# Performance work log

Measured on AMD Instinct MI355X. Metric: run time of the kernel, lower is better.

Reference implementation:

```python
import jax, jax.numpy as jnp
import numpy as np

N = 100000
E = 1600000
IN_DIM = 128
HID_DIM = 128
OUT_DIM = 128


def _gcn_conv(x, W, b, row, col, n):
    # PyG GCNConv: x' = D^{-1/2} (A + I) D^{-1/2} (x W) + b, self-loops included
    xw = x @ W  # [n, dout]
    deg = jnp.zeros((n,), xw.dtype).at[col].add(1.0)  # in-degree incl self-loops
    dinv = jnp.where(deg > 0, jax.lax.rsqrt(deg), 0.0)
    norm = dinv[row] * dinv[col]  # [e]
    msg = xw[row] * norm[:, None]  # [e, dout] -- dominant memory traffic
    out = jax.ops.segment_sum(msg, col, num_segments=n)
    return out + b


def setup_inputs() -> dict:
    key = jax.random.key(0)
    k1, k2, k3, k4, k5, k6 = jax.random.split(key, 6)
    posts = jax.random.normal(k1, (N, IN_DIM), dtype=jnp.float32)
    edge_index = jax.random.randint(k2, (2, E), 0, N, dtype=jnp.int64)
    W1 = jax.random.normal(k3, (IN_DIM, HID_DIM), dtype=jnp.float32) * (1.0 / np.sqrt(IN_DIM))
    b1 = jnp.zeros((HID_DIM,), dtype=jnp.float32)
    W2 = jax.random.normal(k4, (HID_DIM + IN_DIM, OUT_DIM), dtype=jnp.float32) * (1.0 / np.sqrt(HID_DIM + IN_DIM))
    b2 = jnp.zeros((OUT_DIM,), dtype=jnp.float32)
    return {"posts": posts, "W1": W1, "b1": b1, "W2": W2, "b2": b2,
            "edge_index": edge_index, "rootIndex": 0}


def reference(posts, W1, b1, W2, b2, edge_index, rootIndex):
    n = posts.shape[0]
    loops = jnp.arange(n, dtype=edge_index.dtype)
    row = jnp.concatenate([edge_index[0], loops])
    col = jnp.concatenate([edge_index[1], loops])

    conv1_out = _gcn_conv(posts, W1, b1, row, col, n)  # [n, hid]
    post_root = jnp.broadcast_to(posts[rootIndex], (n, posts.shape[1]))
    conv1_root = jnp.broadcast_to(conv1_out[rootIndex], (n, conv1_out.shape[1]))

    conv2_in = jax.nn.relu(jnp.concatenate([conv1_out, post_root], axis=1))
    # dropout is identity at inference
    conv2_out = jax.nn.relu(_gcn_conv(conv2_in, W2, b2, row, col, n))

    feature = jnp.concatenate([conv1_root, conv2_out], axis=1)  # [n, hid+out]
    # avg_pool1d(kernel_size=3, stride=1) over the feature axis -> [n, hid+out-2]
    pooled = (feature[:, :-2] + feature[:, 1:-1] + feature[:, 2:]) * (1.0 / 3.0)
    return pooled
```

## Files before the change

### kernel.cpp

```cpp
#include <hip/hip_runtime.h>
#include <hip/hip_fp16.h>

#define DIM 128
typedef _Float16 half8 __attribute__((ext_vector_type(8)));
typedef float f32x4 __attribute__((ext_vector_type(4)));

__global__ void k_scan1(const int* __restrict__ cnt, int* __restrict__ off,
                        int* __restrict__ bsum, int N){
  __shared__ int s[256];
  int i = blockIdx.x*256 + threadIdx.x;
  int v = (i < N) ? cnt[i] : 0;
  s[threadIdx.x] = v;
  __syncthreads();
  for (int d = 1; d < 256; d <<= 1){
    int t = (threadIdx.x >= d) ? s[threadIdx.x - d] : 0;
    __syncthreads();
    s[threadIdx.x] += t;
    __syncthreads();
  }
  if (i < N) off[i] = s[threadIdx.x] - v;
  if (threadIdx.x == 255) bsum[blockIdx.x] = s[255];
}

__global__ void k_scan2(int* __restrict__ bsum, int nb){
  __shared__ int s[512];
  int t = threadIdx.x;
  int v = (t < nb) ? bsum[t] : 0;
  s[t] = v;
  __syncthreads();
  for (int d = 1; d < 512; d <<= 1){
    int x = (t >= d) ? s[t - d] : 0;
    __syncthreads();
    s[t] += x;
    __syncthreads();
  }
  if (t < nb) bsum[t] = s[t] - v;
}

__global__ void k_scan3(int* __restrict__ off, const int* __restrict__ bsum,
                        const int* __restrict__ cnt, float* __restrict__ dinv,
                        __half* __restrict__ dinvh, int N){
  int i = blockIdx.x*blockDim.x + threadIdx.x;
  if (i < N){
    off[i] += bsum[i >> 8];
    float d = rsqrtf((float)(cnt[i] + 1));
    dinv[i] = d;
    dinvh[i] = __float2half_rn(d);
  }
}

#define NSTRIPE 8
__global__ void k_scatter(const int* __restrict__ row, const int* __restrict__ col,
                          const int* __restrict__ rank, const int* __restrict__ off,
                          int* __restrict__ csr_row, int E, int N){
  int stride = gridDim.x * 256;
  for (int s = 0; s < NSTRIPE; s++){
    int lo = (int)(((long long)s * N) >> 3);
    int hi = (int)(((long long)(s+1) * N) >> 3);
    for (int e = blockIdx.x*256 + threadIdx.x; e < E; e += stride){
      int c = col[e];
      if (c >= lo && c < hi){
        csr_row[off[c] + rank[e]] = row[e];
      }
    }
  }
}

__global__ void k_wprep(const float* __restrict__ Wsrc, __half* __restrict__ Wfh){
  _Float16* Wf = (_Float16*)Wfh;
  int id   = blockIdx.x*256 + threadIdx.x;
  int lane = id & 63;
  int ckc  = id >> 6;
  int kc   = ckc & 3, ct = ckc >> 2;
  int kbase = kc*32 + (lane >> 4)*8;
  int c     = ct*16 + (lane & 15);
  half8 v;
  #pragma unroll
  for (int i = 0; i < 8; i++)
    v[i] = (_Float16)Wsrc[(size_t)(kbase + i)*DIM + c];
  *(half8*)(Wf + (size_t)id*8) = v;
}

template<int INH>
__device__ __forceinline__ void gemm_mfma(const void* __restrict__ Xv,
    const _Float16* __restrict__ Wf, const float* __restrict__ addvec,
    const float* __restrict__ dinv, __half* __restrict__ Yh, int N, int doRelu, int gb){
  int wid = threadIdx.x >> 6;
  int l   = threadIdx.x & 63;
  int g   = l >> 4;
  int lr  = l & 15;
  int rowA = gb*64 + wid*16 + lr;
  int rA   = (rowA < N) ? rowA : (N - 1);

  f32x4 acc[8];
  #pragma unroll
  for (int ct = 0; ct < 8; ct++) acc[ct] = (f32x4){0.f, 0.f, 0.f, 0.f};

  #pragma unroll
  for (int kc = 0; kc < 4; kc++){
    half8 a;
    if (INH){
      a = *(const half8*)((const _Float16*)Xv + (size_t)rA*DIM + kc*32 + g*8);
    } else {
      const float* xp = (const float*)Xv + (size_t)rA*DIM + kc*32 + g*8;
      float4 x0 = *(const float4*)xp;
      float4 x1 = *(const float4*)(xp + 4);
      a[0]=(_Float16)x0.x; a[1]=(_Float16)x0.y; a[2]=(_Float16)x0.z; a[3]=(_Float16)x0.w;
      a[4]=(_Float16)x1.x; a[5]=(_Float16)x1.y; a[6]=(_Float16)x1.z; a[7]=(_Float16)x1.w;
    }
    if (doRelu){
      #pragma unroll
      for (int i = 0; i < 8; i++) a[i] = (a[i] > (_Float16)0.f) ? a[i] : (_Float16)0.f;
    }
    #pragma unroll
    for (int ct = 0; ct < 8; ct++){
      half8 b = *(const half8*)(Wf + ((size_t)(ct*4 + kc)*64 + l)*8);
      acc[ct] = __builtin_amdgcn_mfma_f32_16x16x32_f16(a, b, acc[ct], 0, 0, 0);
    }
  }

  int m0 = gb*64 + wid*16 + g*4;
  float av[8];
  #pragma unroll
  for (int ct = 0; ct < 8; ct++) av[ct] = addvec ? addvec[ct*16 + lr] : 0.f;
  #pragma unroll
  for (int r = 0; r < 4; r++){
    int rr = m0 + r;
    if (rr < N){
      float dv = dinv ? dinv[rr] : 1.f;
      #pragma unroll
      for (int ct = 0; ct < 8; ct++){
        float o = dv*(acc[ct][r] + av[ct]);
        Yh[(size_t)rr*DIM + ct*16 + lr] = __float2half(o);
      }
    }
  }
}

template<int INH>
__global__ __launch_bounds__(256) void k_gemmM(const void* __restrict__ Xv,
    const __half* __restrict__ Wfh, const float* __restrict__ addvec,
    const float* __restrict__ dinv, __half* __restrict__ Yh, int N, int doRelu){
  gemm_mfma<INH>(Xv, (const _Float16*)Wfh, addvec, dinv, Yh, N, doRelu, blockIdx.x);
}

__global__ __launch_bounds__(256) void k_megaA(const float* __restrict__ posts,
    const __half* __restrict__ Wf1, __half* __restrict__ xw1u,
    const int* __restrict__ col, int E, int* __restrict__ cnt, int* __restrict__ rank,
    int N, int nG, int nC){
  int bid = blockIdx.x;
  int m = bid % 5;
  if (m == 4){
    int g = bid / 5;
    if (g < nG)
      gemm_mfma<0>(posts, (const _Float16*)Wf1, nullptr, nullptr, xw1u, N, 0, g);
  } else {
    int c = (bid/5)*4 + m;
    if (c < nC){
      int i = c*256 + threadIdx.x;
      if (i < E) rank[i] = atomicAdd(&cnt[col[i]], 1);
    }
  }
}

__global__ void k_conv1(const __half* __restrict__ xw1u, const int* __restrict__ csr_row,
                        const int* __restrict__ off, const int* __restrict__ cnt,
                        const float* __restrict__ dinv, const __half* __restrict__ dinvh,
                        const float* __restrict__ b, const int* __restrict__ rootIdx,
                        __half* __restrict__ outh, float* __restrict__ c1root, int N){
  int wid  = (blockIdx.x*blockDim.x + threadIdx.x) >> 6;
  if (wid >= N) return;
  int lane = threadIdx.x & 63;
  int half = lane >> 5;
  int sl   = lane & 31;
  int v = wid;
  float dv = dinv[v];
  int o0 = off[v], total = cnt[v] + 1;

  __half2 a01 = __float2half2_rn(0.f), a23 = __float2half2_rn(0.f);
  const __half* base = xw1u;

  auto idx = [&](int t){ return (t == 0) ? v : csr_row[o0 + t - 1]; };
  auto accum = [&](uint2 wv, __half dh){
    __half2 d2 = __half2half2(dh);
    a01 = __hfma2(*(__half2*)&wv.x, d2, a01);
    a23 = __hfma2(*(__half2*)&wv.y, d2, a23);
  };

  int j = half;
  if (j + 14 < total){
    int nid[8];
    #pragma unroll
    for (int q = 0; q < 8; q++) nid[q] = idx(j + 2*q);
    while (j + 14 < total){
      int cur[8];
      #pragma unroll
      for (int q = 0; q < 8; q++) cur[q] = nid[q];
      int jn = j + 16;
      if (jn + 14 < total){
        #pragma unroll
        for (int q = 0; q < 8; q++) nid[q] = csr_row[o0 + jn + 2*q - 1];
      }
      uint2 u[8]; __half dh[8];
      #pragma unroll
      for (int q = 0; q < 8; q++){
        u[q]  = *(const uint2*)(base + (size_t)cur[q]*DIM + sl*4);
        dh[q] = dinvh[cur[q]];
      }
      #pragma unroll
      for (int q = 0; q < 8; q++) accum(u[q], dh[q]);
      j = jn;
    }
  }
  while (j + 6 < total){
    int i0 = idx(j), i1 = idx(j+2), i2 = idx(j+4), i3 = idx(j+6);
    uint2 u0 = *(const uint2*)(base + (size_t)i0*DIM + sl*4);
    uint2 u1 = *(const uint2*)(base + (size_t)i1*DIM + sl*4);
    uint2 u2 = *(const uint2*)(base + (size_t)i2*DIM + sl*4);
    uint2 u3 = *(const uint2*)(base + (size_t)i3*DIM + sl*4);
    __half d0 = dinvh[i0], d1 = dinvh[i1], d2 = dinvh[i2], d3 = dinvh[i3];
    accum(u0, d0); accum(u1, d1); accum(u2, d2); accum(u3, d3);
    j += 8;
  }
  for (; j < total; j += 2){
    int r = idx(j);
    uint2 u = *(const uint2*)(base + (size_t)r*DIM + sl*4);
    accum(u, dinvh[r]);
  }

  int r01 = __shfl_xor(*(int*)&a01, 32);
  int r23 = __shfl_xor(*(int*)&a23, 32);
  a01 = __hadd2(a01, *(__half2*)&r01);
  a23 = __hadd2(a23, *(__half2*)&r23);

  if (half == 0){
    float2 f01 = __half22float2(a01), f23 = __half22float2(a23);
    float4 bb = *(const float4*)(b + sl*4);
    float rx = dv*f01.x + bb.x, ry = dv*f01.y + bb.y;
    float rz = dv*f23.x + bb.z, rw = dv*f23.y + bb.w;
    __half2 h01 = __floats2half2_rn(rx, ry);
    __half2 h23 = __floats2half2_rn(rz, rw);
    uint2 u = make_uint2(*(unsigned int*)&h01, *(unsigned int*)&h23);
    *(uint2*)(outh + (size_t)v*DIM + sl*4) = u;
    if (v == rootIdx[0])
      *(float4*)(c1root + sl*4) = make_float4(rx, ry, rz, rw);
  }
}

__global__ void k_small(const float* __restrict__ posts, const float* __restrict__ W2,
                        const float* __restrict__ c1root, const int* __restrict__ rootIdx,
                        float* __restrict__ cvec, float* __restrict__ cpool){
  int j = threadIdx.x;
  int root = rootIdx[0];
  __shared__ float pr[DIM];
  __shared__ float cr[DIM];
  pr[j] = fmaxf(posts[(size_t)root*DIM + j], 0.f);
  cr[j] = c1root[j];
  __syncthreads();
  float s = 0.f;
  #pragma unroll 4
  for (int k = 0; k < DIM; k++) s += pr[k] * W2[(size_t)(DIM + k)*DIM + j];
  cvec[j] = s;
  cpool[j] = (j < 126) ? (cr[j] + cr[j+1] + cr[j+2]) * (1.f/3.f) : cr[j];
}

__global__ void k_conv2(const __half* __restrict__ xws, const int* __restrict__ csr_row,
                        const int* __restrict__ off, const int* __restrict__ cnt,
                        const float* __restrict__ dinv, const float* __restrict__ b2,
                        const float* __restrict__ cpool, float* __restrict__ out, int N){
  int wid  = (blockIdx.x*blockDim.x + threadIdx.x) >> 6;
  if (wid >= N) return;
  int lane = threadIdx.x & 63;
  int half = lane >> 5;
  int sl   = lane & 31;
  int v = wid;
  float dv = dinv[v];
  int o0 = off[v], total = cnt[v] + 1;

  __half2 a01 = __float2half2_rn(0.f), a23 = __float2half2_rn(0.f);
  const __half* base = xws;

  auto idx = [&](int t){ return (t == 0) ? v : csr_row[o0 + t - 1]; };
  auto accum = [&](uint2 wv){
    a01 = __hadd2(a01, *(__half2*)&wv.x);
    a23 = __hadd2(a23, *(__half2*)&wv.y);
  };

  int j = half;
  if (j + 14 < total){
    int nid[8];
    #pragma unroll
    for (int q = 0; q < 8; q++) nid[q] = idx(j + 2*q);
    while (j + 14 < total){
      int cur[8];
      #pragma unroll
      for (int q = 0; q < 8; q++) cur[q] = nid[q];
      int jn = j + 16;
      if (jn + 14 < total){
        #pragma unroll
        for (int q = 0; q < 8; q++) nid[q] = csr_row[o0 + jn + 2*q - 1];
      }
      uint2 u[8];
      #pragma unroll
      for (int q = 0; q < 8; q++) u[q] = *(const uint2*)(base + (size_t)cur[q]*DIM + sl*4);
      #pragma unroll
      for (int q = 0; q < 8; q++) accum(u[q]);
      j = jn;
    }
  }
  while (j + 6 < total){
    int i0 = idx(j), i1 = idx(j+2), i2 = idx(j+4), i3 = idx(j+6);
    uint2 u0 = *(const uint2*)(base + (size_t)i0*DIM + sl*4);
    uint2 u1 = *(const uint2*)(base + (size_t)i1*DIM + sl*4);
    uint2 u2 = *(const uint2*)(base + (size_t)i2*DIM + sl*4);
    uint2 u3 = *(const uint2*)(base + (size_t)i3*DIM + sl*4);
    accum(u0); accum(u1); accum(u2); accum(u3);
    j += 8;
  }
  for (; j < total; j += 2){
    uint2 u = *(const uint2*)(base + (size_t)idx(j)*DIM + sl*4);
    accum(u);
  }

  int r01 = __shfl_xor(*(int*)&a01, 32);
  int r23 = __shfl_xor(*(int*)&a23, 32);
  a01 = __hadd2(a01, *(__half2*)&r01);
  a23 = __hadd2(a23, *(__half2*)&r23);

  float2 f01 = __half22float2(a01), f23 = __half22float2(a23);
  float4 bb = *(const float4*)(b2 + sl*4);
  float o0v = fmaxf(dv*f01.x + bb.x, 0.f);
  float o1v = fmaxf(dv*f01.y + bb.y, 0.f);
  float o2v = fmaxf(dv*f23.x + bb.z, 0.f);
  float o3v = fmaxf(dv*f23.y + bb.w, 0.f);

  float pz = __shfl_up(o2v, 1);
  float pw = __shfl_up(o3v, 1);
  if (sl == 0){ pz = cpool[126]; pw = cpool[127]; }
  const float third = 1.f/3.f;
  float q0 = (pz + pw + o0v) * third;
  float q1 = (pw + o0v + o1v) * third;
  float q2 = (o0v + o1v + o2v) * third;
  float q3 = (o1v + o2v + o3v) * third;

  float* orow = out + (size_t)v*254;
  if (half == 0){
    *(float2*)(orow + 126 + sl*4)     = make_float2(q0, q1);
    *(float2*)(orow + 126 + sl*4 + 2) = make_float2(q2, q3);
  } else {
    if (sl < 31) *(float4*)(orow + sl*4) = *(const float4*)(cpool + sl*4);
    else         *(float2*)(orow + 124)  = *(const float2*)(cpool + 124);
  }
}

extern "C" void kernel_launch(void* const* d_in, const int* in_sizes, int n_in,
                              void* d_out, int out_size, void* d_ws, size_t ws_size,
                              hipStream_t stream){
  const float* posts = (const float*)d_in[0];
  const float* W1    = (const float*)d_in[1];
  const float* b1    = (const float*)d_in[2];
  const float* W2    = (const float*)d_in[3];
  const float* b2    = (const float*)d_in[4];
  const int*   eidx  = (const int*)d_in[5];
  const int*   rootI = (const int*)d_in[6];
  int N = in_sizes[0] / DIM;
  int E = in_sizes[5] / 2;
  const int* row = eidx;
  const int* col = eidx + E;

  char* p = (char*)d_ws;
  auto alloc = [&](size_t bytes)->void*{
    void* q = (void*)p; p += (bytes + 255) & ~(size_t)255; return q;
  };
  __half* xw1u  = (__half*)alloc((size_t)N*DIM*2);
  __half* xw2s  = (__half*)alloc((size_t)N*DIM*2);
  __half* c1h   = (__half*)alloc((size_t)N*DIM*2);
  __half* Wf1   = (__half*)alloc((size_t)DIM*DIM*2);
  __half* Wf2   = (__half*)alloc((size_t)DIM*DIM*2);
  __half* dinvh = (__half*)alloc((size_t)N*2);
  float* dinv   = (float*)alloc((size_t)N*4);
  float* c1root = (float*)alloc(DIM*4);
  float* cvec   = (float*)alloc(DIM*4);
  float* cpool  = (float*)alloc(DIM*4);
  int*   cnt    = (int*)alloc((size_t)N*4);
  int*   off    = (int*)alloc((size_t)N*4);
  int*   rank   = (int*)alloc((size_t)E*4);
  int*   bsum   = (int*)alloc(512*4);
  int*   csrrow = (int*)alloc((size_t)E*4);

  hipMemsetAsync(cnt, 0, (size_t)N*4, stream);

  int nb = (N + 255) / 256;
  int nG = (N + 63) / 64;
  int nC = (E + 255) / 256;
  int q5 = nG > (nC + 3)/4 ? nG : (nC + 3)/4;

  k_wprep<<<8, 256, 0, stream>>>(W1, Wf1);
  k_wprep<<<8, 256, 0, stream>>>(W2, Wf2);
  k_megaA<<<5*q5, 256, 0, stream>>>(posts, Wf1, xw1u, col, E, cnt, rank, N, nG, nC);
  k_scan1<<<nb, 256, 0, stream>>>(cnt, off, bsum, N);
  k_scan2<<<1, 512, 0, stream>>>(bsum, nb);
  k_scan3<<<nb, 256, 0, stream>>>(off, bsum, cnt, dinv, dinvh, N);
  k_scatter<<<2048, 256, 0, stream>>>(row, col, rank, off, csrrow, E, N);

  k_conv1<<<(N + 3)/4, 256, 0, stream>>>(xw1u, csrrow, off, cnt, dinv, dinvh, b1, rootI,
                                         c1h, c1root, N);
  k_small<<<1, 128, 0, stream>>>(posts, W2, c1root, rootI, cvec, cpool);
  k_gemmM<1><<<(N + 63)/64, 256, 0, stream>>>(c1h, Wf2, cvec, dinv, xw2s, N, 1);
  k_conv2<<<(N + 3)/4, 256, 0, stream>>>(xw2s, csrrow, off, cnt, dinv, b2, cpool,
                                         (float*)d_out, N);
}
```

Measured before the change: 293.9 us.

## Fuse layer-1 GEMM with CSR scatter instead of with degree counting

Separates the atomic degree count into its own kernel and moves the first-layer MFMA GEMM into a combined kernel with the CSR scatter. The idea is to overlap the compute-bound GEMM with the memory-bound scatter rather than with the atomics, so the GEMM blocks come first and the scatter blocks fill in around them. The scatter also drops from 8 column stripes to 4, cutting passes over the edge list but giving each pass a wider write window and less locality. The count kernel now stands alone on the critical path.

```diff
diff --git a/kernel.cpp b/kernel.cpp
--- a/kernel.cpp
+++ b/kernel.cpp
@@ -4,6 +4,12 @@
 #define DIM 128
 typedef _Float16 half8 __attribute__((ext_vector_type(8)));
 typedef float f32x4 __attribute__((ext_vector_type(4)));
+
+__global__ void k_count(const int* __restrict__ col, int E,
+                        int* __restrict__ cnt, int* __restrict__ rank){
+  int i = blockIdx.x*blockDim.x + threadIdx.x;
+  if (i < E) rank[i] = atomicAdd(&cnt[col[i]], 1);
+}
 
 __global__ void k_scan1(const int* __restrict__ cnt, int* __restrict__ off,
                         int* __restrict__ bsum, int N){
@@ -46,23 +52,6 @@
     float d = rsqrtf((float)(cnt[i] + 1));
     dinv[i] = d;
     dinvh[i] = __float2half_rn(d);
-  }
-}
-
-#define NSTRIPE 8
-__global__ void k_scatter(const int* __restrict__ row, const int* __restrict__ col,
-                          const int* __restrict__ rank, const int* __restrict__ off,
-                          int* __restrict__ csr_row, int E, int N){
-  int stride = gridDim.x * 256;
-  for (int s = 0; s < NSTRIPE; s++){
-    int lo = (int)(((long long)s * N) >> 3);
-    int hi = (int)(((long long)(s+1) * N) >> 3);
-    for (int e = blockIdx.x*256 + threadIdx.x; e < E; e += stride){
-      int c = col[e];
-      if (c >= lo && c < hi){
-        csr_row[off[c] + rank[e]] = row[e];
-      }
-    }
   }
 }
 
@@ -144,21 +133,28 @@
   gemm_mfma<INH>(Xv, (const _Float16*)Wfh, addvec, dinv, Yh, N, doRelu, blockIdx.x);
 }
 
-__global__ __launch_bounds__(256) void k_megaA(const float* __restrict__ posts,
+#define NSTRIPE 4
+__global__ __launch_bounds__(256) void k_megaB(const float* __restrict__ posts,
     const __half* __restrict__ Wf1, __half* __restrict__ xw1u,
-    const int* __restrict__ col, int E, int* __restrict__ cnt, int* __restrict__ rank,
-    int N, int nG, int nC){
+    const int* __restrict__ row, const int* __restrict__ col,
+    const int* __restrict__ rank, const int* __restrict__ off,
+    int* __restrict__ csr_row, int E, int N, int nG, int nS){
   int bid = blockIdx.x;
-  int m = bid % 5;
-  if (m == 4){
-    int g = bid / 5;
-    if (g < nG)
-      gemm_mfma<0>(posts, (const _Float16*)Wf1, nullptr, nullptr, xw1u, N, 0, g);
+  if (bid < nG){
+    gemm_mfma<0>(posts, (const _Float16*)Wf1, nullptr, nullptr, xw1u, N, 0, bid);
   } else {
-    int c = (bid/5)*4 + m;
-    if (c < nC){
-      int i = c*256 + threadIdx.x;
-      if (i < E) rank[i] = atomicAdd(&cnt[col[i]], 1);
+    int sb = bid - nG;
+    int stride = nS * 256;
+    #pragma unroll 1
+    for (int s = 0; s < NSTRIPE; s++){
+      int lo = (int)(((long long)s * N) / NSTRIPE);
+      int hi = (int)(((long long)(s+1) * N) / NSTRIPE);
+      for (int e = sb*256 + threadIdx.x; e < E; e += stride){
+        int c = col[e];
+        if (c >= lo && c < hi){
+          csr_row[off[c] + rank[e]] = row[e];
+        }
+      }
     }
   }
 }
@@ -392,16 +388,16 @@
 
   int nb = (N + 255) / 256;
   int nG = (N + 63) / 64;
-  int nC = (E + 255) / 256;
-  int q5 = nG > (nC + 3)/4 ? nG : (nC + 3)/4;
+  int nS = 2048;
 
   k_wprep<<<8, 256, 0, stream>>>(W1, Wf1);
   k_wprep<<<8, 256, 0, stream>>>(W2, Wf2);
-  k_megaA<<<5*q5, 256, 0, stream>>>(posts, Wf1, xw1u, col, E, cnt, rank, N, nG, nC);
+  k_count<<<(E + 255)/256, 256, 0, stream>>>(col, E, cnt, rank);
   k_scan1<<<nb, 256, 0, stream>>>(cnt, off, bsum, N);
   k_scan2<<<1, 512, 0, stream>>>(bsum, nb);
   k_scan3<<<nb, 256, 0, stream>>>(off, bsum, cnt, dinv, dinvh, N);
-  k_scatter<<<2048, 256, 0, stream>>>(row, col, rank, off, csrrow, E, N);
+  k_megaB<<<nG + nS, 256, 0, stream>>>(posts, Wf1, xw1u, row, col, rank, off,
+                                       csrrow, E, N, nG, nS);
 
   k_conv1<<<(N + 3)/4, 256, 0, stream>>>(xw1u, csrrow, off, cnt, dinv, dinvh, b1, rootI,
                                          c1h, c1root, N);
```

After: 309.7 us. +5.4%, slower.

## Cache scatter positions, merge weight prep, move constant pooled columns into GEMM kernel

Applied to the files above, without the earlier changes.

The CSR scatter now computes each edge's destination position once, stores it in a new pos buffer, and filters later stripes by position range instead of re-reading col, off and rank. The two weight-prep launches are merged into one. Writing the constant first 126 output columns (cpool) moves out of conv2 into extra blocks of a new combined kernel alongside the second GEMM. This trades an extra E-sized buffer and a less coalesced column fill for fewer launches and less per-stripe gather traffic, and it shortens conv2's epilogue.

```diff
diff --git a/kernel.cpp b/kernel.cpp
--- a/kernel.cpp
+++ b/kernel.cpp
@@ -52,23 +52,33 @@
 #define NSTRIPE 8
 __global__ void k_scatter(const int* __restrict__ row, const int* __restrict__ col,
                           const int* __restrict__ rank, const int* __restrict__ off,
-                          int* __restrict__ csr_row, int E, int N){
+                          int* __restrict__ pos, int* __restrict__ csr_row, int E, int N){
   int stride = gridDim.x * 256;
-  for (int s = 0; s < NSTRIPE; s++){
-    int lo = (int)(((long long)s * N) >> 3);
-    int hi = (int)(((long long)(s+1) * N) >> 3);
-    for (int e = blockIdx.x*256 + threadIdx.x; e < E; e += stride){
-      int c = col[e];
-      if (c >= lo && c < hi){
-        csr_row[off[c] + rank[e]] = row[e];
-      }
-    }
-  }
-}
-
-__global__ void k_wprep(const float* __restrict__ Wsrc, __half* __restrict__ Wfh){
-  _Float16* Wf = (_Float16*)Wfh;
-  int id   = blockIdx.x*256 + threadIdx.x;
+  int tid0 = blockIdx.x*256 + threadIdx.x;
+  int hi0  = (int)(((long long)1 * N) / NSTRIPE);
+  int pHi0 = off[hi0];
+  for (int e = tid0; e < E; e += stride){
+    int p = off[col[e]] + rank[e];
+    pos[e] = p;
+    if (p < pHi0) csr_row[p] = row[e];
+  }
+  for (int s = 1; s < NSTRIPE; s++){
+    int lo = (int)(((long long)s * N) / NSTRIPE);
+    int hi = (int)(((long long)(s+1) * N) / NSTRIPE);
+    int pLo = off[lo];
+    int pHi = (s == NSTRIPE-1) ? E : off[hi];
+    for (int e = tid0; e < E; e += stride){
+      int p = pos[e];
+      if (p >= pLo && p < pHi) csr_row[p] = row[e];
+    }
+  }
+}
+
+__global__ void k_wprep(const float* __restrict__ W1, const float* __restrict__ W2,
+                        __half* __restrict__ Wf1h, __half* __restrict__ Wf2h){
+  const float* Wsrc = (blockIdx.x < 8) ? W1 : W2;
+  _Float16* Wf = (_Float16*)((blockIdx.x < 8) ? Wf1h : Wf2h);
+  int id   = (blockIdx.x & 7)*256 + threadIdx.x;
   int lane = id & 63;
   int ckc  = id >> 6;
   int kc   = ckc & 3, ct = ckc >> 2;
@@ -135,13 +145,6 @@
       }
     }
   }
-}
-
-template<int INH>
-__global__ __launch_bounds__(256) void k_gemmM(const void* __restrict__ Xv,
-    const __half* __restrict__ Wfh, const float* __restrict__ addvec,
-    const float* __restrict__ dinv, __half* __restrict__ Yh, int N, int doRelu){
-  gemm_mfma<INH>(Xv, (const _Float16*)Wfh, addvec, dinv, Yh, N, doRelu, blockIdx.x);
 }
 
 __global__ __launch_bounds__(256) void k_megaA(const float* __restrict__ posts,
@@ -163,6 +166,30 @@
   }
 }
 
+__global__ __launch_bounds__(256) void k_megaC(const __half* __restrict__ c1h,
+    const __half* __restrict__ Wf2, const float* __restrict__ cvec,
+    const float* __restrict__ dinv, __half* __restrict__ xw2s,
+    const float* __restrict__ cpool, float* __restrict__ outp, int N, int nG, int nF){
+  int bid = blockIdx.x;
+  if (bid < nG){
+    gemm_mfma<1>(c1h, (const _Float16*)Wf2, cvec, dinv, xw2s, N, 1, bid);
+  } else {
+    int f = bid - nG;
+    if (f >= nF) return;
+    int total = N * 63;
+    #pragma unroll
+    for (int i = 0; i < 8; i++){
+      int w = f*2048 + i*256 + threadIdx.x;
+      if (w < total){
+        unsigned int r  = (unsigned int)w / 63u;
+        unsigned int c2 = (unsigned int)w - r*63u;
+        float2 val = *(const float2*)(cpool + c2*2);
+        *(float2*)(outp + (size_t)r*254 + c2*2) = val;
+      }
+    }
+  }
+}
+
 __global__ void k_conv1(const __half* __restrict__ xw1u, const int* __restrict__ csr_row,
                         const int* __restrict__ off, const int* __restrict__ cnt,
                         const float* __restrict__ dinv, const __half* __restrict__ dinvh,
@@ -327,29 +354,26 @@
   a01 = __hadd2(a01, *(__half2*)&r01);
   a23 = __hadd2(a23, *(__half2*)&r23);
 
-  float2 f01 = __half22float2(a01), f23 = __half22float2(a23);
-  float4 bb = *(const float4*)(b2 + sl*4);
-  float o0v = fmaxf(dv*f01.x + bb.x, 0.f);
-  float o1v = fmaxf(dv*f01.y + bb.y, 0.f);
-  float o2v = fmaxf(dv*f23.x + bb.z, 0.f);
-  float o3v = fmaxf(dv*f23.y + bb.w, 0.f);
-
-  float pz = __shfl_up(o2v, 1);
-  float pw = __shfl_up(o3v, 1);
-  if (sl == 0){ pz = cpool[126]; pw = cpool[127]; }
-  const float third = 1.f/3.f;
-  float q0 = (pz + pw + o0v) * third;
-  float q1 = (pw + o0v + o1v) * third;
-  float q2 = (o0v + o1v + o2v) * third;
-  float q3 = (o1v + o2v + o3v) * third;
-
-  float* orow = out + (size_t)v*254;
   if (half == 0){
+    float2 f01 = __half22float2(a01), f23 = __half22float2(a23);
+    float4 bb = *(const float4*)(b2 + sl*4);
+    float o0v = fmaxf(dv*f01.x + bb.x, 0.f);
+    float o1v = fmaxf(dv*f01.y + bb.y, 0.f);
+    float o2v = fmaxf(dv*f23.x + bb.z, 0.f);
+    float o3v = fmaxf(dv*f23.y + bb.w, 0.f);
+
+    float pz = __shfl_up(o2v, 1);
+    float pw = __shfl_up(o3v, 1);
+    if (sl == 0){ pz = cpool[126]; pw = cpool[127]; }
+    const float third = 1.f/3.f;
+    float q0 = (pz + pw + o0v) * third;
+    float q1 = (pw + o0v + o1v) * third;
+    float q2 = (o0v + o1v + o2v) * third;
+    float q3 = (o1v + o2v + o3v) * third;
+
+    float* orow = out + (size_t)v*254;
     *(float2*)(orow + 126 + sl*4)     = make_float2(q0, q1);
     *(float2*)(orow + 126 + sl*4 + 2) = make_float2(q2, q3);
-  } else {
-    if (sl < 31) *(float4*)(orow + sl*4) = *(const float4*)(cpool + sl*4);
-    else         *(float2*)(orow + 124)  = *(const float2*)(cpool + 124);
   }
 }
 
@@ -385,6 +409,7 @@
   int*   cnt    = (int*)alloc((size_t)N*4);
   int*   off    = (int*)alloc((size_t)N*4);
   int*   rank   = (int*)alloc((size_t)E*4);
+  int*   pos    = (int*)alloc((size_t)E*4);
   int*   bsum   = (int*)alloc(512*4);
   int*   csrrow = (int*)alloc((size_t)E*4);
 
@@ -394,19 +419,20 @@
   int nG = (N + 63) / 64;
   int nC = (E + 255) / 256;
   int q5 = nG > (nC + 3)/4 ? nG : (nC + 3)/4;
-
-  k_wprep<<<8, 256, 0, stream>>>(W1, Wf1);
-  k_wprep<<<8, 256, 0, stream>>>(W2, Wf2);
+  int nF = (N*63 + 2047) / 2048;
+
+  k_wprep<<<16, 256, 0, stream>>>(W1, W2, Wf1, Wf2);
   k_megaA<<<5*q5, 256, 0, stream>>>(posts, Wf1, xw1u, col, E, cnt, rank, N, nG, nC);
   k_scan1<<<nb, 256, 0, stream>>>(cnt, off, bsum, N);
   k_scan2<<<1, 512, 0, stream>>>(bsum, nb);
   k_scan3<<<nb, 256, 0, stream>>>(off, bsum, cnt, dinv, dinvh, N);
-  k_scatter<<<2048, 256, 0, stream>>>(row, col, rank, off, csrrow, E, N);
+  k_scatter<<<2048, 256, 0, stream>>>(row, col, rank, off, pos, csrrow, E, N);
 
   k_conv1<<<(N + 3)/4, 256, 0, stream>>>(xw1u, csrrow, off, cnt, dinv, dinvh, b1, rootI,
                                          c1h, c1root, N);
   k_small<<<1, 128, 0, stream>>>(posts, W2, c1root, rootI, cvec, cpool);
-  k_gemmM<1><<<(N + 63)/64, 256, 0, stream>>>(c1h, Wf2, cvec, dinv, xw2s, N, 1);
+  k_megaC<<<nG + nF, 256, 0, stream>>>(c1h, Wf2, cvec, dinv, xw2s, cpool,
+                                       (float*)d_out, N, nG, nF);
   k_conv2<<<(N + 3)/4, 256, 0, stream>>>(xw2s, csrrow, off, cnt, dinv, b2, cpool,
                                          (float*)d_out, N);
 }
```

Result: no change. 298.0 us (+1.4%).
